# Kernel optimization log

Hardware: AMD Instinct MI355X
Metric: run time of the kernel (lower is better)

Reference implementation:

```python
import math
import jax, jax.numpy as jnp
import numpy as np

EMB = 1024
HEADS = 16
HEAD_DIM = EMB // HEADS
FF = 4 * EMB
EPS = 1e-5


def gelu_tanh(x):
    c = math.sqrt(2.0 / math.pi)
    return 0.5 * x * (1.0 + jnp.tanh(c * (x + 0.044715 * x ** 3)))


def layernorm(x, scale, shift):
    mean = jnp.mean(x, axis=-1, keepdims=True)
    var = jnp.var(x, axis=-1, keepdims=True)
    return scale * (x - mean) / jnp.sqrt(var + EPS) + shift


def setup_inputs() -> dict:
    key = jax.random.key(0)
    ks = jax.random.split(key, 10)
    s = 0.02
    return {
        "x": jax.random.normal(ks[0], (2, 2048, EMB), dtype=jnp.float32),
        "Wq": jax.random.normal(ks[1], (EMB, EMB), dtype=jnp.float32) * s,
        "Wk": jax.random.normal(ks[2], (EMB, EMB), dtype=jnp.float32) * s,
        "Wv": jax.random.normal(ks[3], (EMB, EMB), dtype=jnp.float32) * s,
        "Wo": jax.random.normal(ks[4], (EMB, EMB), dtype=jnp.float32) * s,
        "bo": jnp.zeros((EMB,), dtype=jnp.float32),
        "W1": jax.random.normal(ks[5], (EMB, FF), dtype=jnp.float32) * s,
        "b1": jnp.zeros((FF,), dtype=jnp.float32),
        "W2": jax.random.normal(ks[6], (FF, EMB), dtype=jnp.float32) * s,
        "b2": jnp.zeros((EMB,), dtype=jnp.float32),
        "ln1_scale": jnp.ones((EMB,), dtype=jnp.float32),
        "ln1_shift": jnp.zeros((EMB,), dtype=jnp.float32),
        "ln2_scale": jnp.ones((EMB,), dtype=jnp.float32),
        "ln2_shift": jnp.zeros((EMB,), dtype=jnp.float32),
    }


def reference(x, Wq, Wk, Wv, Wo, bo, W1, b1, W2, b2,
              ln1_scale, ln1_shift, ln2_scale, ln2_shift):
    B, S, D = x.shape
    # --- pre-LN causal MHA ---
    h = layernorm(x, ln1_scale, ln1_shift)
    q = (h @ Wq).reshape(B, S, HEADS, HEAD_DIM).transpose(0, 2, 1, 3)  # [B,H,S,d]
    k = (h @ Wk).reshape(B, S, HEADS, HEAD_DIM).transpose(0, 2, 1, 3)
    v = (h @ Wv).reshape(B, S, HEADS, HEAD_DIM).transpose(0, 2, 1, 3)
    scores = jnp.einsum("bhqd,bhkd->bhqk", q, k)  # [B,H,S,S]
    causal = jnp.triu(jnp.ones((S, S), dtype=bool), k=1)
    scores = jnp.where(causal, -jnp.inf, scores)
    attn = jax.nn.softmax(scores / math.sqrt(HEAD_DIM), axis=-1)
    ctx = jnp.einsum("bhqk,bhkd->bhqd", attn, v)  # [B,H,S,d]
    ctx = ctx.transpose(0, 2, 1, 3).reshape(B, S, D)
    x = x + (ctx @ Wo + bo)
    # --- FFN ---
    h = layernorm(x, ln2_scale, ln2_shift)
    h = gelu_tanh(h @ W1 + b1) @ W2 + b2
    return x + h
```

## Files before the change

### kernel.cpp

```cpp
#include <hip/hip_runtime.h>
#include <hip/hip_bf16.h>
#include <math.h>

#define EMB 1024
#define HEADS 16
#define HEAD_DIM 64
#define FF_DIM 4096
#define SEQ 2048
#define BATCH 2
#define NTOK (BATCH * SEQ)
#define LN_EPS 1e-5f
#define QKV_N 3072
#define Q_PRESCALE 0.18033688011112042f

typedef __attribute__((ext_vector_type(8))) short s8v;
typedef __attribute__((ext_vector_type(4))) float f4v;

__device__ __forceinline__ unsigned short f2bf(float f) {
    union { __hip_bfloat16 h; unsigned short u; } cv;
    cv.h = __float2bfloat16(f);
    return cv.u;
}

__device__ __forceinline__ float fast_exp2(float x) {
#if __has_builtin(__builtin_amdgcn_exp2f)
    return __builtin_amdgcn_exp2f(x);
#else
    return exp2f(x);
#endif
}

__device__ __forceinline__ float gelu_f(float x) {
    const float c = 0.7978845608028654f;
    float x3 = x * x * x;
    return 0.5f * x * (1.0f + tanhf(c * (x + 0.044715f * x3)));
}

#define GLDS(gp, lp)                                                        \
    __builtin_amdgcn_global_load_lds(                                       \
        (const __attribute__((address_space(1))) void*)(gp),                \
        (__attribute__((address_space(3))) void*)(lp), 16, 0, 0)

#define BAR()   do { __builtin_amdgcn_s_barrier(); __builtin_amdgcn_sched_barrier(0); } while (0)
#define LGKM0() do { asm volatile("s_waitcnt lgkmcnt(0)" ::: "memory"); __builtin_amdgcn_sched_barrier(0); } while (0)
#define VMCNT(n) do { asm volatile("s_waitcnt vmcnt(" #n ")" ::: "memory"); __builtin_amdgcn_sched_barrier(0); } while (0)

__global__ __launch_bounds__(256) void ln_bf16_kernel(const float* __restrict__ x,
                                                      const float* __restrict__ scale,
                                                      const float* __restrict__ shift,
                                                      unsigned short* __restrict__ out) {
    int row = blockIdx.x;
    int tid = threadIdx.x;
    const float4 xv = ((const float4*)(x + (size_t)row * EMB))[tid];
    float s  = xv.x + xv.y + xv.z + xv.w;
    float ss = xv.x * xv.x + xv.y * xv.y + xv.z * xv.z + xv.w * xv.w;
    __shared__ float2 red[256];
    red[tid] = make_float2(s, ss);
    __syncthreads();
    for (int off = 128; off > 0; off >>= 1) {
        if (tid < off) {
            red[tid].x += red[tid + off].x;
            red[tid].y += red[tid + off].y;
        }
        __syncthreads();
    }
    float mean = red[0].x * (1.0f / EMB);
    float var  = red[0].y * (1.0f / EMB) - mean * mean;
    float rstd = rsqrtf(var + LN_EPS);
    float4 sc4 = ((const float4*)scale)[tid];
    float4 sh4 = ((const float4*)shift)[tid];
    ushort4 o;
    o.x = f2bf(sc4.x * (xv.x - mean) * rstd + sh4.x);
    o.y = f2bf(sc4.y * (xv.y - mean) * rstd + sh4.y);
    o.z = f2bf(sc4.z * (xv.z - mean) * rstd + sh4.z);
    o.w = f2bf(sc4.w * (xv.w - mean) * rstd + sh4.w);
    *(ushort4*)(out + (size_t)row * EMB + tid * 4) = o;
}

__device__ __forceinline__ void tconv_tile(const float* __restrict__ W,
                                           unsigned short* __restrict__ Wt,
                                           int K, int N, int bx, int by, int tid) {
    __shared__ float t[64][65];
    int n0 = bx * 64, k0 = by * 64;
#pragma unroll
    for (int it = 0; it < 4; ++it) {
        int f = tid + it * 256;
        int r = f >> 4, c = (f & 15) * 4;
        float4 w = *(const float4*)(W + (size_t)(k0 + r) * N + n0 + c);
        t[r][c] = w.x; t[r][c + 1] = w.y; t[r][c + 2] = w.z; t[r][c + 3] = w.w;
    }
    __syncthreads();
#pragma unroll
    for (int it = 0; it < 4; ++it) {
        int f = tid + it * 256;
        int rn = f >> 4, ck = (f & 15) * 4;
        ushort4 o;
        o.x = f2bf(t[ck + 0][rn]);
        o.y = f2bf(t[ck + 1][rn]);
        o.z = f2bf(t[ck + 2][rn]);
        o.w = f2bf(t[ck + 3][rn]);
        *(ushort4*)(Wt + (size_t)(n0 + rn) * K + k0 + ck) = o;
    }
}

__global__ __launch_bounds__(256) void tconv_all_kernel(
    const float* __restrict__ Wq, const float* __restrict__ Wk,
    const float* __restrict__ Wv, const float* __restrict__ Wo,
    const float* __restrict__ W1, const float* __restrict__ W2,
    unsigned short* __restrict__ Wqkv_t, unsigned short* __restrict__ Wo_t,
    unsigned short* __restrict__ W1_t, unsigned short* __restrict__ W2_t) {
    int b = blockIdx.x;
    int tid = threadIdx.x;
    if (b < 256)        tconv_tile(Wq, Wqkv_t,                      EMB, EMB,    b & 15, b >> 4, tid);
    else if (b < 512)   tconv_tile(Wk, Wqkv_t + (size_t)1024 * EMB, EMB, EMB,    (b - 256) & 15, (b - 256) >> 4, tid);
    else if (b < 768)   tconv_tile(Wv, Wqkv_t + (size_t)2048 * EMB, EMB, EMB,    (b - 512) & 15, (b - 512) >> 4, tid);
    else if (b < 1024)  tconv_tile(Wo, Wo_t,                        EMB, EMB,    (b - 768) & 15, (b - 768) >> 4, tid);
    else if (b < 2048)  tconv_tile(W1, W1_t,                        EMB, FF_DIM, (b - 1024) & 63, (b - 1024) >> 6, tid);
    else                tconv_tile(W2, W2_t,                        FF_DIM, EMB, (b - 2048) & 15, (b - 2048) >> 4, tid);
}

__global__ __launch_bounds__(256) void reduce_kernel(const float* __restrict__ p0,
                                                     const float* __restrict__ p1,
                                                     const float* __restrict__ bias,
                                                     const float* __restrict__ residual,
                                                     float* __restrict__ out) {
    size_t i4 = ((size_t)blockIdx.x * 256 + threadIdx.x) * 4;
    float4 a = *(const float4*)(p0 + i4);
    float4 b = *(const float4*)(p1 + i4);
    float4 r = *(const float4*)(residual + i4);
    int col = (int)(i4 & (EMB - 1));
    float4 bs = *(const float4*)(bias + col);
    float4 o;
    o.x = a.x + b.x + r.x + bs.x;
    o.y = a.y + b.y + r.y + bs.y;
    o.z = a.z + b.z + r.z + bs.z;
    o.w = a.w + b.w + r.w + bs.w;
    *(float4*)(out + i4) = o;
}

__global__ __launch_bounds__(256) void reduce_ln_kernel(const float* __restrict__ p0,
                                                        const float* __restrict__ p1,
                                                        const float* __restrict__ bias,
                                                        const float* __restrict__ residual,
                                                        float* __restrict__ x1,
                                                        const float* __restrict__ scale,
                                                        const float* __restrict__ shift,
                                                        unsigned short* __restrict__ out) {
    int row = blockIdx.x;
    int tid = threadIdx.x;
    size_t i4 = (size_t)row * EMB + tid * 4;
    float4 a = *(const float4*)(p0 + i4);
    float4 b = *(const float4*)(p1 + i4);
    float4 r = *(const float4*)(residual + i4);
    float4 bs = *(const float4*)(bias + tid * 4);
    float4 xv;
    xv.x = a.x + b.x + r.x + bs.x;
    xv.y = a.y + b.y + r.y + bs.y;
    xv.z = a.z + b.z + r.z + bs.z;
    xv.w = a.w + b.w + r.w + bs.w;
    *(float4*)(x1 + i4) = xv;

    float s  = xv.x + xv.y + xv.z + xv.w;
    float ss = xv.x * xv.x + xv.y * xv.y + xv.z * xv.z + xv.w * xv.w;
    __shared__ float2 red[256];
    red[tid] = make_float2(s, ss);
    __syncthreads();
    for (int off = 128; off > 0; off >>= 1) {
        if (tid < off) {
            red[tid].x += red[tid + off].x;
            red[tid].y += red[tid + off].y;
        }
        __syncthreads();
    }
    float mean = red[0].x * (1.0f / EMB);
    float var  = red[0].y * (1.0f / EMB) - mean * mean;
    float rstd = rsqrtf(var + LN_EPS);
    float4 sc4 = ((const float4*)scale)[tid];
    float4 sh4 = ((const float4*)shift)[tid];
    ushort4 o;
    o.x = f2bf(sc4.x * (xv.x - mean) * rstd + sh4.x);
    o.y = f2bf(sc4.y * (xv.y - mean) * rstd + sh4.y);
    o.z = f2bf(sc4.z * (xv.z - mean) * rstd + sh4.z);
    o.w = f2bf(sc4.w * (xv.w - mean) * rstd + sh4.w);
    *(ushort4*)(out + i4) = o;
}

__global__ __launch_bounds__(256) void gemm_fused_kernel(
    const unsigned short* __restrict__ A,
    const unsigned short* __restrict__ Bt,
    unsigned short* __restrict__ Cb,
    int M, int N, int K,
    const float* __restrict__ bias,
    int do_gelu, int qkv_mode,
    unsigned short* __restrict__ vt)
{
    __shared__ short lds[16384];
    short* As = lds;
    short* Bs = lds + 8192;

    int tid = threadIdx.x;
    int nbx = N >> 7, nby8 = (M >> 7) >> 3;
    int bid = (int)blockIdx.x;
    int xcd = bid & 7;
    int t   = bid >> 3;
    int x   = t % nbx;
    int u   = t / nbx;
    int y   = (u % nby8) * 8 + xcd;
    int m0 = y << 7, n0 = x << 7;

    int wv = tid >> 6, lane = tid & 63;
    int wr = wv >> 1, wc = wv & 1;
    int quad = lane >> 4, ln = lane & 15;

    f4v acc[4][4];
#pragma unroll
    for (int i = 0; i < 4; ++i)
#pragma unroll
        for (int j = 0; j < 4; ++j) { f4v z4 = {0.f, 0.f, 0.f, 0.f}; acc[i][j] = z4; }

    int r0 = tid & 127;
    size_t Kby = (size_t)K << 1;
    const char* Ag0 = (const char*)A + (size_t)(m0 + r0) * Kby + (size_t)((tid >> 7) << 4);
    const char* Bg0 = (const char*)Bt + (size_t)(n0 + r0) * Kby + (size_t)((tid >> 7) << 4);

    int nIter = K >> 5;
    GLDS(Ag0, (char*)As + tid * 16);
    GLDS(Ag0 + 32, (char*)As + tid * 16 + 4096);
    GLDS(Bg0, (char*)Bs + tid * 16);
    GLDS(Bg0 + 32, (char*)Bs + tid * 16 + 4096);

    for (int it = 0; it < nIter; ++it) {
        VMCNT(0);
        BAR();
        if (it + 1 < nIter) {
            int kb = (it + 1) << 6;
            char* Ad = (char*)As + ((it + 1) & 1) * 8192 + tid * 16;
            char* Bd = (char*)Bs + ((it + 1) & 1) * 8192 + tid * 16;
            GLDS(Ag0 + kb, Ad);
            GLDS(Ag0 + kb + 32, Ad + 4096);
            GLDS(Bg0 + kb, Bd);
            GLDS(Bg0 + kb + 32, Bd + 4096);
            __builtin_amdgcn_sched_barrier(0);
        }
        const short* Ab = As + (it & 1) * 4096;
        const short* Bb = Bs + (it & 1) * 4096;
        s8v af[4], bfr[4];
#pragma unroll
        for (int i = 0; i < 4; ++i)
            af[i] = *(const s8v*)(Ab + ((size_t)quad * 128 + wr * 64 + i * 16 + ln) * 8);
#pragma unroll
        for (int j = 0; j < 4; ++j)
            bfr[j] = *(const s8v*)(Bb + ((size_t)quad * 128 + wc * 64 + j * 16 + ln) * 8);
#pragma unroll
        for (int i = 0; i < 4; ++i)
#pragma unroll
            for (int j = 0; j < 4; ++j)
                acc[i][j] = __builtin_amdgcn_mfma_f32_16x16x32_bf16(af[i], bfr[j], acc[i][j], 0, 0, 0);
    }

    LGKM0();
    BAR();

    int colb = wc * 64 + ln;
    int rowb = wr * 64 + quad * 4;
    int off8 = (tid & 15) * 8;
    int sub  = tid >> 4;

    if (qkv_mode && n0 >= 2048) {
#pragma unroll
        for (int j = 0; j < 4; ++j) {
            int c = colb + j * 16;
            int swz = (c & 7) << 3;
#pragma unroll
            for (int i = 0; i < 4; ++i) {
                int rw = rowb + i * 16;
                ushort4 pk;
                pk.x = f2bf(acc[i][j][0]);
                pk.y = f2bf(acc[i][j][1]);
                pk.z = f2bf(acc[i][j][2]);
                pk.w = f2bf(acc[i][j][3]);
                *(ushort4*)(lds + c * 128 + (rw ^ swz)) = pk;
            }
        }
        BAR();
        int bb = m0 >> 11, s0b = m0 & 2047;
        size_t vbase = ((size_t)bb * 1024 + (n0 - 2048)) * SEQ + s0b + off8;
#pragma unroll
        for (int pass = 0; pass < 8; ++pass) {
            int c = pass * 16 + sub;
            s8v v = *(const s8v*)(lds + c * 128 + (off8 ^ ((c & 7) << 3)));
            *(s8v*)(vt + vbase + (size_t)c * SEQ) = v;
        }
        return;
    }

    bool isq = qkv_mode && (n0 < 1024);
#pragma unroll
    for (int j = 0; j < 4; ++j) {
        int c = colb + j * 16;
        float bj = (!qkv_mode && bias) ? bias[n0 + c] : 0.f;
#pragma unroll
        for (int i = 0; i < 4; ++i) {
            int rw = rowb + i * 16;
#pragma unroll
            for (int r = 0; r < 4; ++r) {
                float vv = acc[i][j][r];
                if (qkv_mode) { if (isq) vv *= Q_PRESCALE; }
                else { vv += bj; if (do_gelu) vv = gelu_f(vv); }
                int rr_ = rw + r;
                lds[rr_ * 128 + (c ^ ((rr_ & 7) << 3))] = (short)f2bf(vv);
            }
        }
    }
    BAR();
    int ldc = qkv_mode ? 2048 : N;
#pragma unroll
    for (int pass = 0; pass < 8; ++pass) {
        int rw = pass * 16 + sub;
        s8v v = *(const s8v*)(lds + rw * 128 + (off8 ^ ((rw & 7) << 3)));
        *(s8v*)(Cb + (size_t)(m0 + rw) * ldc + n0 + off8) = v;
    }
}

__global__ __launch_bounds__(256) void gemm_bf16_kernel(
    const unsigned short* __restrict__ A,
    const unsigned short* __restrict__ Bt,
    float* __restrict__ Cf0,
    float* __restrict__ Cf1,
    int M, int N, int K, int Klen)
{
    __shared__ short As[2][4096];
    __shared__ short Bs[2][4096];

    int tid = threadIdx.x;
    int nbx = N >> 7, nby8 = (M >> 7) >> 3;
    int bid = (int)blockIdx.x;
    int xcd = bid & 7;
    int t   = bid >> 3;
    int x   = t % nbx;
    int u   = t / nbx;
    int y   = (u % nby8) * 8 + xcd;
    int z   = u / nby8;

    int m0 = y << 7;
    int n0 = x << 7;
    int k0 = z * Klen;
    float* Cf = z ? Cf1 : Cf0;
    int wv = tid >> 6, lane = tid & 63;
    int wr = wv >> 1, wc = wv & 1;
    int quad = lane >> 4, ln = lane & 15;

    f4v acc[4][4];
#pragma unroll
    for (int i = 0; i < 4; ++i)
#pragma unroll
        for (int j = 0; j < 4; ++j) {
            f4v z4 = {0.f, 0.f, 0.f, 0.f};
            acc[i][j] = z4;
        }

    int r0 = tid & 127;
    size_t Kby = (size_t)K << 1;
    const char* Ag0 = (const char*)A + (size_t)(m0 + r0) * Kby + (size_t)k0 * 2 + (tid >> 7) * 16;
    const char* Bg0 = (const char*)Bt + (size_t)(n0 + r0) * Kby + (size_t)k0 * 2 + (tid >> 7) * 16;

    int nIter = Klen >> 5;
    GLDS(Ag0, (char*)As[0] + tid * 16);
    GLDS(Ag0 + 32, (char*)As[0] + tid * 16 + 4096);
    GLDS(Bg0, (char*)Bs[0] + tid * 16);
    GLDS(Bg0 + 32, (char*)Bs[0] + tid * 16 + 4096);

    for (int it = 0; it < nIter; ++it) {
        VMCNT(0);
        BAR();
        if (it + 1 < nIter) {
            int kb = (it + 1) << 6;
            char* Ad = (char*)As[(it + 1) & 1] + tid * 16;
            char* Bd = (char*)Bs[(it + 1) & 1] + tid * 16;
            GLDS(Ag0 + kb, Ad);
            GLDS(Ag0 + kb + 32, Ad + 4096);
            GLDS(Bg0 + kb, Bd);
            GLDS(Bg0 + kb + 32, Bd + 4096);
            __builtin_amdgcn_sched_barrier(0);
        }
        const short* Ab = As[it & 1];
        const short* Bb = Bs[it & 1];
        s8v af[4], bfr[4];
#pragma unroll
        for (int i = 0; i < 4; ++i)
            af[i] = *(const s8v*)(Ab + ((size_t)quad * 128 + wr * 64 + i * 16 + ln) * 8);
#pragma unroll
        for (int j = 0; j < 4; ++j)
            bfr[j] = *(const s8v*)(Bb + ((size_t)quad * 128 + wc * 64 + j * 16 + ln) * 8);
#pragma unroll
        for (int i = 0; i < 4; ++i)
#pragma unroll
            for (int j = 0; j < 4; ++j)
                acc[i][j] = __builtin_amdgcn_mfma_f32_16x16x32_bf16(af[i], bfr[j], acc[i][j], 0, 0, 0);
    }

    int cn  = n0 + wc * 64 + ln;
    int cm0 = m0 + wr * 64 + quad * 4;
#pragma unroll
    for (int j = 0; j < 4; ++j) {
        int gn = cn + j * 16;
#pragma unroll
        for (int i = 0; i < 4; ++i)
#pragma unroll
            for (int r = 0; r < 4; ++r)
                Cf[(size_t)(cm0 + i * 16 + r) * N + gn] = acc[i][j][r];
    }
}

__global__ __launch_bounds__(256) void flash_attn_mfma_kernel(
    const unsigned short* __restrict__ qk,
    const unsigned short* __restrict__ vt,
    unsigned short* __restrict__ ctx)
{
    int h  = blockIdx.x;
    int b  = blockIdx.z;
    int qt = b ? (int)blockIdx.y : ((int)gridDim.y - 1 - (int)blockIdx.y);
    int tid = threadIdx.x;
    int w = tid >> 6, lane = tid & 63;
    int quad = lane >> 4, ln = lane & 15;

    __shared__ short Kb2[2][4096];
    __shared__ short Vb2[2][4096];
    __shared__ short Ps[4][32 * 72];

    size_t qrow0 = (size_t)b * SEQ + (size_t)qt * 128;
    int wrow0 = w * 32;

    s8v qf[2][2];
#pragma unroll
    for (int mb = 0; mb < 2; ++mb)
#pragma unroll
        for (int ks = 0; ks < 2; ++ks)
            qf[mb][ks] = *(const s8v*)(qk + (qrow0 + wrow0 + mb * 16 + ln) * 2048
                                          + h * 64 + ks * 32 + quad * 8);

    float l_part[2][4];
    f4v o[2][4];
#pragma unroll
    for (int mb = 0; mb < 2; ++mb) {
#pragma unroll
        for (int r = 0; r < 4; ++r) l_part[mb][r] = 0.f;
#pragma unroll
        for (int db = 0; db < 4; ++db) {
            f4v z = {0.f, 0.f, 0.f, 0.f};
            o[mb][db] = z;
        }
    }

    const unsigned short* kb_p = qk + (size_t)b * SEQ * 2048 + 1024 + h * 64;
    const unsigned short* vb_p = vt + ((size_t)b * 1024 + h * 64) * SEQ;
    short* Pw = Ps[w];

    int rr = tid & 63;
    const unsigned short* Kg0 = kb_p + (size_t)rr * 2048 + (tid >> 6) * 8;
    const unsigned short* Vg0 = vb_p + (size_t)rr * 2048 + (tid >> 6) * 8;

    int ktn = 2 * qt + 2;
    int ktmax_w = (qt * 128 + wrow0 + 31) >> 6;

    GLDS(Kg0, (char*)Kb2[0] + tid * 16);
    GLDS(Kg0 + 32, (char*)Kb2[0] + tid * 16 + 4096);
    GLDS(Vg0, (char*)Vb2[0] + tid * 16);
    GLDS(Vg0 + 32, (char*)Vb2[0] + tid * 16 + 4096);

    for (int kt = 0; kt < ktn; ++kt) {
        BAR();
        bool pf = (kt + 1 < ktn);
        if (pf) {
            int nb_ = (kt + 1) & 1;
            const unsigned short* ks_ = Kg0 + (size_t)(kt + 1) * 64 * 2048;
            const unsigned short* vs_ = Vg0 + (kt + 1) * 64;
            GLDS(ks_, (char*)Kb2[nb_] + tid * 16);
            GLDS(ks_ + 32, (char*)Kb2[nb_] + tid * 16 + 4096);
            GLDS(vs_, (char*)Vb2[nb_] + tid * 16);
            GLDS(vs_ + 32, (char*)Vb2[nb_] + tid * 16 + 4096);
        }
        if (kt > ktmax_w) continue;
        if (pf) { VMCNT(8); } else { VMCNT(0); }

        const short* Kl = Kb2[kt & 1];
        const short* Vl = Vb2[kt & 1];

        f4v s[2][4];
#pragma unroll
        for (int mb = 0; mb < 2; ++mb)
#pragma unroll
            for (int nb = 0; nb < 4; ++nb) {
                f4v z = {0.f, 0.f, 0.f, 0.f};
                s[mb][nb] = z;
            }
#pragma unroll
        for (int ks = 0; ks < 2; ++ks)
#pragma unroll
            for (int nb = 0; nb < 4; ++nb) {
                s8v kfr = *(const s8v*)(Kl + ((size_t)(ks * 4 + quad) * 64 + nb * 16 + ln) * 8);
#pragma unroll
                for (int mb = 0; mb < 2; ++mb)
                    s[mb][nb] = __builtin_amdgcn_mfma_f32_16x16x32_bf16(qf[mb][ks], kfr, s[mb][nb], 0, 0, 0);
            }

        bool edge = (kt == ktmax_w);
#pragma unroll
        for (int mb = 0; mb < 2; ++mb) {
#pragma unroll
            for (int r = 0; r < 4; ++r) {
                int rloc = mb * 16 + quad * 4 + r;
                float p[4];
                if (!edge) {
#pragma unroll
                    for (int nb = 0; nb < 4; ++nb)
                        p[nb] = fast_exp2(s[mb][nb][r]);
                } else {
                    int grow = qt * 128 + wrow0 + rloc;
#pragma unroll
                    for (int nb = 0; nb < 4; ++nb) {
                        int key = kt * 64 + nb * 16 + ln;
                        float e = fast_exp2(s[mb][nb][r]);
                        p[nb] = (key > grow) ? 0.f : e;
                    }
                }
                l_part[mb][r] += (p[0] + p[1]) + (p[2] + p[3]);
#pragma unroll
                for (int nb = 0; nb < 4; ++nb)
                    Pw[rloc * 72 + nb * 16 + ln] = f2bf(p[nb]);
            }
        }

#pragma unroll
        for (int ks = 0; ks < 2; ++ks) {
            s8v pf_[2];
#pragma unroll
            for (int mb = 0; mb < 2; ++mb)
                pf_[mb] = *(const s8v*)(Pw + (mb * 16 + ln) * 72 + ks * 32 + quad * 8);
#pragma unroll
            for (int db = 0; db < 4; ++db) {
                s8v vfr = *(const s8v*)(Vl + ((size_t)(ks * 4 + quad) * 64 + db * 16 + ln) * 8);
#pragma unroll
                for (int mb = 0; mb < 2; ++mb)
                    o[mb][db] = __builtin_amdgcn_mfma_f32_16x16x32_bf16(pf_[mb], vfr, o[mb][db], 0, 0, 0);
            }
        }
    }

    asm volatile("s_waitcnt vmcnt(0)" ::: "memory");

#pragma unroll
    for (int mb = 0; mb < 2; ++mb)
#pragma unroll
        for (int r = 0; r < 4; ++r) {
            float l = l_part[mb][r];
#pragma unroll
            for (int msk = 1; msk < 16; msk <<= 1)
                l += __shfl_xor(l, msk);
            float inv = 1.0f / l;
            size_t row = qrow0 + wrow0 + mb * 16 + quad * 4 + r;
#pragma unroll
            for (int db = 0; db < 4; ++db)
                ctx[row * EMB + h * 64 + db * 16 + ln] = f2bf(o[mb][db][r] * inv);
        }
}

extern "C" void kernel_launch(void* const* d_in, const int* in_sizes, int n_in,
                              void* d_out, int out_size, void* d_ws, size_t ws_size,
                              hipStream_t stream) {
    const float* x    = (const float*)d_in[0];
    const float* Wq   = (const float*)d_in[1];
    const float* Wk   = (const float*)d_in[2];
    const float* Wv   = (const float*)d_in[3];
    const float* Wo   = (const float*)d_in[4];
    const float* bo   = (const float*)d_in[5];
    const float* W1   = (const float*)d_in[6];
    const float* b1   = (const float*)d_in[7];
    const float* W2   = (const float*)d_in[8];
    const float* b2   = (const float*)d_in[9];
    const float* ln1s = (const float*)d_in[10];
    const float* ln1b = (const float*)d_in[11];
    const float* ln2s = (const float*)d_in[12];
    const float* ln2b = (const float*)d_in[13];
    float* out = (float*)d_out;

    const size_t MiB = 1024 * 1024;
    uint8_t* w8 = (uint8_t*)d_ws;
    unsigned short* Wqkv_t = (unsigned short*)(w8);
    unsigned short* Wo_t   = (unsigned short*)(w8 +  6 * MiB);
    unsigned short* W1_t   = (unsigned short*)(w8 +  8 * MiB);
    unsigned short* W2_t   = (unsigned short*)(w8 + 16 * MiB);
    unsigned short* act_bf = (unsigned short*)(w8 + 24 * MiB);
    unsigned short* qk_bf  = (unsigned short*)(w8 + 32 * MiB);
    unsigned short* vt     = (unsigned short*)(w8 + 48 * MiB);
    float*          p0a    = (float*)(w8 + 32 * MiB);
    float*          p1a    = (float*)(w8 + 48 * MiB);
    unsigned short* u_bf   = (unsigned short*)(w8 + 32 * MiB);
    float*          x1     = (float*)(w8 + 64 * MiB);
    float*          p0b    = (float*)(w8);
    float*          p1b    = (float*)(w8 + 80 * MiB);

    tconv_all_kernel<<<3072, 256, 0, stream>>>(Wq, Wk, Wv, Wo, W1, W2,
                                               Wqkv_t, Wo_t, W1_t, W2_t);

    ln_bf16_kernel<<<NTOK, 256, 0, stream>>>(x, ln1s, ln1b, act_bf);

    gemm_fused_kernel<<<(NTOK / 128) * (QKV_N / 128), 256, 0, stream>>>(
        act_bf, Wqkv_t, qk_bf, NTOK, QKV_N, EMB, nullptr, 0, 1, vt);

    flash_attn_mfma_kernel<<<dim3(HEADS, SEQ / 128, BATCH), 256, 0, stream>>>(qk_bf, vt, act_bf);

    gemm_bf16_kernel<<<(EMB / 128) * (NTOK / 128) * 2, 256, 0, stream>>>(
        act_bf, Wo_t, p0a, p1a, NTOK, EMB, EMB, 512);
    reduce_ln_kernel<<<NTOK, 256, 0, stream>>>(p0a, p1a, bo, x, x1, ln2s, ln2b, act_bf);

    gemm_fused_kernel<<<(NTOK / 128) * (FF_DIM / 128), 256, 0, stream>>>(
        act_bf, W1_t, u_bf, NTOK, FF_DIM, EMB, b1, 1, 0, nullptr);

    gemm_bf16_kernel<<<(EMB / 128) * (NTOK / 128) * 2, 256, 0, stream>>>(
        u_bf, W2_t, p0b, p1b, NTOK, EMB, FF_DIM, 2048);
    reduce_kernel<<<(NTOK * EMB) / 1024, 256, 0, stream>>>(p0b, p1b, b2, x1, out);
}
```

Measured before the change: 474.9 us.

## Triple-buffer GEMM LDS staging and use exp2-based tanh in GELU

Both bf16 GEMM kernels move from double to triple buffering of the A/B tiles in LDS. Loads are issued two iterations ahead and the wait is relaxed to vmcnt(4), so global-to-LDS latency overlaps more with MFMA work. The GELU epilogue replaces tanhf with a fast exp2 formulation of tanh. The trade-offs are more shared memory per block, which may lower occupancy, and slightly different GELU rounding.

```diff
diff --git a/kernel.cpp b/kernel.cpp
--- a/kernel.cpp
+++ b/kernel.cpp
@@ -32,8 +32,10 @@
 
 __device__ __forceinline__ float gelu_f(float x) {
     const float c = 0.7978845608028654f;
-    float x3 = x * x * x;
-    return 0.5f * x * (1.0f + tanhf(c * (x + 0.044715f * x3)));
+    float y = c * (x + 0.044715f * x * x * x);
+    float e = fast_exp2(y * 2.8853900817779268f);
+    float t = 1.0f - 2.0f / (e + 1.0f);
+    return 0.5f * x * (1.0f + t);
 }
 
 #define GLDS(gp, lp)                                                        \
@@ -194,9 +196,9 @@
     int do_gelu, int qkv_mode,
     unsigned short* __restrict__ vt)
 {
-    __shared__ short lds[16384];
+    __shared__ short lds[24576];
     short* As = lds;
-    short* Bs = lds + 8192;
+    short* Bs = lds + 12288;
 
     int tid = threadIdx.x;
     int nbx = N >> 7, nby8 = (M >> 7) >> 3;
@@ -223,27 +225,27 @@
     const char* Ag0 = (const char*)A + (size_t)(m0 + r0) * Kby + (size_t)((tid >> 7) << 4);
     const char* Bg0 = (const char*)Bt + (size_t)(n0 + r0) * Kby + (size_t)((tid >> 7) << 4);
 
+#define STAGE(tt, bi) do {                                                  \
+    int kb_ = (tt) << 6;                                                    \
+    char* Ad_ = (char*)As + (bi) * 8192 + tid * 16;                         \
+    char* Bd_ = (char*)Bs + (bi) * 8192 + tid * 16;                         \
+    GLDS(Ag0 + kb_, Ad_); GLDS(Ag0 + kb_ + 32, Ad_ + 4096);                 \
+    GLDS(Bg0 + kb_, Bd_); GLDS(Bg0 + kb_ + 32, Bd_ + 4096); } while (0)
+
     int nIter = K >> 5;
-    GLDS(Ag0, (char*)As + tid * 16);
-    GLDS(Ag0 + 32, (char*)As + tid * 16 + 4096);
-    GLDS(Bg0, (char*)Bs + tid * 16);
-    GLDS(Bg0 + 32, (char*)Bs + tid * 16 + 4096);
-
+    STAGE(0, 0);
+    STAGE(1, 1);
+
+    int cur = 0, stg = 2;
     for (int it = 0; it < nIter; ++it) {
-        VMCNT(0);
+        if (it + 1 < nIter) { VMCNT(4); } else { VMCNT(0); }
         BAR();
-        if (it + 1 < nIter) {
-            int kb = (it + 1) << 6;
-            char* Ad = (char*)As + ((it + 1) & 1) * 8192 + tid * 16;
-            char* Bd = (char*)Bs + ((it + 1) & 1) * 8192 + tid * 16;
-            GLDS(Ag0 + kb, Ad);
-            GLDS(Ag0 + kb + 32, Ad + 4096);
-            GLDS(Bg0 + kb, Bd);
-            GLDS(Bg0 + kb + 32, Bd + 4096);
+        if (it + 2 < nIter) {
+            STAGE(it + 2, stg);
             __builtin_amdgcn_sched_barrier(0);
         }
-        const short* Ab = As + (it & 1) * 4096;
-        const short* Bb = Bs + (it & 1) * 4096;
+        const short* Ab = As + cur * 4096;
+        const short* Bb = Bs + cur * 4096;
         s8v af[4], bfr[4];
 #pragma unroll
         for (int i = 0; i < 4; ++i)
@@ -256,7 +258,10 @@
 #pragma unroll
             for (int j = 0; j < 4; ++j)
                 acc[i][j] = __builtin_amdgcn_mfma_f32_16x16x32_bf16(af[i], bfr[j], acc[i][j], 0, 0, 0);
-    }
+        cur = (cur == 2) ? 0 : cur + 1;
+        stg = (stg == 2) ? 0 : stg + 1;
+    }
+#undef STAGE
 
     LGKM0();
     BAR();
@@ -329,8 +334,8 @@
     float* __restrict__ Cf1,
     int M, int N, int K, int Klen)
 {
-    __shared__ short As[2][4096];
-    __shared__ short Bs[2][4096];
+    __shared__ short As[3][4096];
+    __shared__ short Bs[3][4096];
 
     int tid = threadIdx.x;
     int nbx = N >> 7, nby8 = (M >> 7) >> 3;
@@ -364,27 +369,27 @@
     const char* Ag0 = (const char*)A + (size_t)(m0 + r0) * Kby + (size_t)k0 * 2 + (tid >> 7) * 16;
     const char* Bg0 = (const char*)Bt + (size_t)(n0 + r0) * Kby + (size_t)k0 * 2 + (tid >> 7) * 16;
 
+#define STAGE(tt, bi) do {                                                  \
+    int kb_ = (tt) << 6;                                                    \
+    char* Ad_ = (char*)As[bi] + tid * 16;                                   \
+    char* Bd_ = (char*)Bs[bi] + tid * 16;                                   \
+    GLDS(Ag0 + kb_, Ad_); GLDS(Ag0 + kb_ + 32, Ad_ + 4096);                 \
+    GLDS(Bg0 + kb_, Bd_); GLDS(Bg0 + kb_ + 32, Bd_ + 4096); } while (0)
+
     int nIter = Klen >> 5;
-    GLDS(Ag0, (char*)As[0] + tid * 16);
-    GLDS(Ag0 + 32, (char*)As[0] + tid * 16 + 4096);
-    GLDS(Bg0, (char*)Bs[0] + tid * 16);
-    GLDS(Bg0 + 32, (char*)Bs[0] + tid * 16 + 4096);
-
+    STAGE(0, 0);
+    STAGE(1, 1);
+
+    int cur = 0, stg = 2;
     for (int it = 0; it < nIter; ++it) {
-        VMCNT(0);
+        if (it + 1 < nIter) { VMCNT(4); } else { VMCNT(0); }
         BAR();
-        if (it + 1 < nIter) {
-            int kb = (it + 1) << 6;
-            char* Ad = (char*)As[(it + 1) & 1] + tid * 16;
-            char* Bd = (char*)Bs[(it + 1) & 1] + tid * 16;
-            GLDS(Ag0 + kb, Ad);
-            GLDS(Ag0 + kb + 32, Ad + 4096);
-            GLDS(Bg0 + kb, Bd);
-            GLDS(Bg0 + kb + 32, Bd + 4096);
+        if (it + 2 < nIter) {
+            STAGE(it + 2, stg);
             __builtin_amdgcn_sched_barrier(0);
         }
-        const short* Ab = As[it & 1];
-        const short* Bb = Bs[it & 1];
+        const short* Ab = As[cur];
+        const short* Bb = Bs[cur];
         s8v af[4], bfr[4];
 #pragma unroll
         for (int i = 0; i < 4; ++i)
@@ -397,7 +402,10 @@
 #pragma unroll
             for (int j = 0; j < 4; ++j)
                 acc[i][j] = __builtin_amdgcn_mfma_f32_16x16x32_bf16(af[i], bfr[j], acc[i][j], 0, 0, 0);
-    }
+        cur = (cur == 2) ? 0 : cur + 1;
+        stg = (stg == 2) ? 0 : stg + 1;
+    }
+#undef STAGE
 
     int cn  = n0 + wc * 64 + ln;
     int cm0 = m0 + wr * 64 + quad * 4;
```

Result: faster. 442.9 us (-6.7%).
